# Optimization experiments

Measured on AMD Instinct MI355X. Metric: run time of the kernel, lower is better.

## Reference

```python
import jax, jax.numpy as jnp
import numpy as np

H = 64  # hidden size

def _lstm_last_h(x, W_ih, W_hh, b_ih, b_hh):
    # x: [B, T]; PyTorch LSTM gate order: i, f, g, o (each H wide in 4H axis)
    B, T = x.shape
    # input_size == 1, so x @ W_ih.T == x[..., None] * W_ih[:, 0]
    xproj = x[:, :, None] * W_ih[:, 0][None, None, :] + (b_ih + b_hh)  # [B, T, 4H]
    xproj_t = jnp.swapaxes(xproj, 0, 1)  # [T, B, 4H] for scan over time

    def step(carry, xp_t):
        h, c = carry
        gates = xp_t + h @ W_hh.T  # [B, 4H]
        i = jax.nn.sigmoid(gates[:, 0 * H:1 * H])
        f = jax.nn.sigmoid(gates[:, 1 * H:2 * H])
        g = jnp.tanh(gates[:, 2 * H:3 * H])
        o = jax.nn.sigmoid(gates[:, 3 * H:4 * H])
        c = f * c + i * g
        h = o * jnp.tanh(c)
        return (h, c), None

    h0 = jnp.zeros((B, H), x.dtype)
    c0 = jnp.zeros((B, H), x.dtype)
    (h_last, _), _ = jax.lax.scan(step, (h0, c0), xproj_t)
    return h_last  # [B, H] == lstm_out[:, -1, :]


def setup_inputs() -> dict:
    key = jax.random.key(0)
    ks = jax.random.split(key, 7)
    B, T = 2048, 512
    s_ih = 1.0 / np.sqrt(H)
    return {
        "x": jax.random.normal(ks[0], (B, T), jnp.float32),
        "W_ih": jax.random.uniform(ks[1], (4 * H, 1), jnp.float32, -s_ih, s_ih),
        "W_hh": jax.random.uniform(ks[2], (4 * H, H), jnp.float32, -s_ih, s_ih),
        "b_ih": jax.random.uniform(ks[3], (4 * H,), jnp.float32, -s_ih, s_ih),
        "b_hh": jax.random.uniform(ks[4], (4 * H,), jnp.float32, -s_ih, s_ih),
        "W_d": jax.random.uniform(ks[5], (1, H), jnp.float32, -s_ih, s_ih),
        "b_d": jax.random.uniform(ks[6], (1,), jnp.float32, -s_ih, s_ih),
    }


def reference(x, W_ih, W_hh, b_ih, b_hh, W_d, b_d):
    h_last = _lstm_last_h(x, W_ih, W_hh, b_ih, b_hh)  # [B, H]
    out = h_last @ W_d.T + b_d  # [B, 1]
    return out[:, 0]  # squeeze(1) -> [B]
```

## Files before the change

kernel.cpp:

```cpp
#include <hip/hip_runtime.h>

#define TLEN 512
#define HID  64

typedef _Float16 half8 __attribute__((ext_vector_type(8)));
typedef float    f32x4 __attribute__((ext_vector_type(4)));

__device__ __forceinline__ float rcp_fast(float x) { return __builtin_amdgcn_rcpf(x); }
__device__ __forceinline__ float sigmoid_fast(float x) { return rcp_fast(1.0f + __expf(-x)); }
__device__ __forceinline__ float tanh_fast(float x) { return 1.0f - 2.0f * rcp_fast(__expf(2.0f * x) + 1.0f); }

__global__ __launch_bounds__(512)
void lstm_mfma3(const float* __restrict__ x,
                const float* __restrict__ W_ih,
                const float* __restrict__ W_hh,
                const float* __restrict__ b_ih,
                const float* __restrict__ b_hh,
                const float* __restrict__ W_d,
                const float* __restrict__ b_d,
                float* __restrict__ out) {
    __shared__ __align__(16) float    xs[8][516];
    __shared__ __align__(16) _Float16 hbuf[2][16][72];

    const int tid = threadIdx.x;
    const int L   = tid & 63;
    const int w   = tid >> 6;
    const int r0  = blockIdx.x * 8;

    for (int i = tid; i < 8 * 128; i += 512) {
        const int r = i >> 7, t4 = (i & 127) * 4;
        *(float4*)&xs[r][t4] = *(const float4*)&x[(size_t)(r0 + r) * TLEN + t4];
    }
    for (int i = tid; i < 2 * 16 * 72; i += 512)
        ((_Float16*)hbuf)[i] = (_Float16)0.0f;

    half8 af[2][2];
    {
        const int m = L & 15;
        const int g = m & 3;
        const int kb = (L >> 4) * 8;
#pragma unroll
        for (int tt = 0; tt < 2; ++tt) {
            const int uu = 8 * w + 4 * tt + (m >> 2);
            const float* row = &W_hh[(size_t)(g * HID + uu) * HID];
#pragma unroll
            for (int q = 0; q < 2; ++q) {
                const float* p = row + 32 * q + kb;
                half8 hf;
#pragma unroll
                for (int i = 0; i < 8; ++i) hf[i] = (_Float16)p[i];
                af[tt][q] = hf;
            }
        }
    }

    const int c   = L & 15;
    const int b   = L & 7;
    const int sel = (L >> 3) & 1;
    const int u   = 8 * w + (L >> 4) + 4 * sel;

    float wih[4], bias[4];
#pragma unroll
    for (int g = 0; g < 4; ++g) {
        wih[g]  = W_ih[g * HID + u];
        bias[g] = b_ih[g * HID + u] + b_hh[g * HID + u];
    }

    const float* xrow = &xs[b][0];
    _Float16* hw0 = &hbuf[1][b][u];
    const f32x4 zero = {0.0f, 0.0f, 0.0f, 0.0f};
    float cst = 0.0f;
    int p = 0;

    __syncthreads();

    for (int t = 0; t < TLEN; ++t) {
        const _Float16* hb = &hbuf[p][c][(L >> 4) * 8];
        const float xt = xrow[t];
        half8 b0 = *(const half8*)hb;
        half8 b1 = *(const half8*)(hb + 32);

        f32x4 d0 = __builtin_amdgcn_mfma_f32_16x16x32_f16(af[0][0], b0, zero, 0, 0, 0);
        f32x4 d1 = __builtin_amdgcn_mfma_f32_16x16x32_f16(af[1][0], b0, zero, 0, 0, 0);
        d0 = __builtin_amdgcn_mfma_f32_16x16x32_f16(af[0][1], b1, d0, 0, 0, 0);
        d1 = __builtin_amdgcn_mfma_f32_16x16x32_f16(af[1][1], b1, d1, 0, 0, 0);

        const f32x4 d = sel ? d1 : d0;

        const float ai = d[0] + fmaf(xt, wih[0], bias[0]);
        const float af_ = d[1] + fmaf(xt, wih[1], bias[1]);
        const float ag = d[2] + fmaf(xt, wih[2], bias[2]);
        const float ao = d[3] + fmaf(xt, wih[3], bias[3]);
        const float gi = sigmoid_fast(ai);
        const float gf = sigmoid_fast(af_);
        const float gg = tanh_fast(ag);
        const float go = sigmoid_fast(ao);
        cst = fmaf(gf, cst, gi * gg);
        const float hv = go * tanh_fast(cst);

        const _Float16 hh = (_Float16)hv;
        _Float16* hwp = hw0 + (p ^ 1) * 0 ;
        hbuf[p ^ 1][b][u]     = hh;
        hbuf[p ^ 1][b + 8][u] = hh;
        __syncthreads();
        p ^= 1;
    }

    float pv = (float)hbuf[p][w][L] * W_d[L];
#pragma unroll
    for (int off = 32; off > 0; off >>= 1)
        pv += __shfl_xor(pv, off, 64);
    if (L == 0)
        out[r0 + w] = pv + b_d[0];
}

extern "C" void kernel_launch(void* const* d_in, const int* in_sizes, int n_in,
                              void* d_out, int out_size, void* d_ws, size_t ws_size,
                              hipStream_t stream) {
    const float* x    = (const float*)d_in[0];
    const float* W_ih = (const float*)d_in[1];
    const float* W_hh = (const float*)d_in[2];
    const float* b_ih = (const float*)d_in[3];
    const float* b_hh = (const float*)d_in[4];
    const float* W_d  = (const float*)d_in[5];
    const float* b_d  = (const float*)d_in[6];
    float* out = (float*)d_out;

    dim3 grid(256);
    dim3 block(512);
    lstm_mfma3<<<grid, block, 0, stream>>>(x, W_ih, W_hh, b_ih, b_hh, W_d, b_d, out);
}
```

Measured before the change: 234.2 us.

## Split LSTM batch into 4-row blocks of 4 waves with 16 units each

Each block now handles 4 batch rows with 256 threads (4 waves), and each wave owns 16 hidden units using four MFMA tiles per step instead of two. The grid doubles to 512 blocks, so each __syncthreads in the serial time loop covers fewer waves, and the MFMA B tiles are no longer padded with duplicated rows. The time loop is unrolled by two with fixed ping-pong buffer pointers, which removes the buffer-index arithmetic. The cost is more MFMA work per wave and more register pressure, and a waves-per-eu hint is added to bound occupancy.

```diff
diff --git a/kernel.cpp b/kernel.cpp
--- a/kernel.cpp
+++ b/kernel.cpp
@@ -10,8 +10,8 @@
 __device__ __forceinline__ float sigmoid_fast(float x) { return rcp_fast(1.0f + __expf(-x)); }
 __device__ __forceinline__ float tanh_fast(float x) { return 1.0f - 2.0f * rcp_fast(__expf(2.0f * x) + 1.0f); }
 
-__global__ __launch_bounds__(512)
-void lstm_mfma3(const float* __restrict__ x,
+__global__ __launch_bounds__(256) __attribute__((amdgpu_waves_per_eu(2, 2)))
+void lstm_mfma4(const float* __restrict__ x,
                 const float* __restrict__ W_ih,
                 const float* __restrict__ W_hh,
                 const float* __restrict__ b_ih,
@@ -19,29 +19,29 @@
                 const float* __restrict__ W_d,
                 const float* __restrict__ b_d,
                 float* __restrict__ out) {
-    __shared__ __align__(16) float    xs[8][516];
-    __shared__ __align__(16) _Float16 hbuf[2][16][72];
+    __shared__ __align__(16) float    xs[4][516];
+    __shared__ __align__(16) _Float16 hbuf[2][4][72];
 
     const int tid = threadIdx.x;
     const int L   = tid & 63;
     const int w   = tid >> 6;
-    const int r0  = blockIdx.x * 8;
+    const int r0  = blockIdx.x * 4;
 
-    for (int i = tid; i < 8 * 128; i += 512) {
+    for (int i = tid; i < 4 * 128; i += 256) {
         const int r = i >> 7, t4 = (i & 127) * 4;
         *(float4*)&xs[r][t4] = *(const float4*)&x[(size_t)(r0 + r) * TLEN + t4];
     }
-    for (int i = tid; i < 2 * 16 * 72; i += 512)
+    for (int i = tid; i < 2 * 4 * 72; i += 256)
         ((_Float16*)hbuf)[i] = (_Float16)0.0f;
 
-    half8 af[2][2];
+    half8 af[4][2];
     {
         const int m = L & 15;
         const int g = m & 3;
         const int kb = (L >> 4) * 8;
 #pragma unroll
-        for (int tt = 0; tt < 2; ++tt) {
-            const int uu = 8 * w + 4 * tt + (m >> 2);
+        for (int tt = 0; tt < 4; ++tt) {
+            const int uu = 16 * w + 4 * tt + (m >> 2);
             const float* row = &W_hh[(size_t)(g * HID + uu) * HID];
 #pragma unroll
             for (int q = 0; q < 2; ++q) {
@@ -54,10 +54,9 @@
         }
     }
 
-    const int c   = L & 15;
-    const int b   = L & 7;
-    const int sel = (L >> 3) & 1;
-    const int u   = 8 * w + (L >> 4) + 4 * sel;
+    const int b   = L & 3;
+    const int sel = (L >> 2) & 3;
+    const int u   = 16 * w + 4 * sel + (L >> 4);
 
     float wih[4], bias[4];
 #pragma unroll
@@ -67,46 +66,52 @@
     }
 
     const float* xrow = &xs[b][0];
-    _Float16* hw0 = &hbuf[1][b][u];
+    const int koff = (L >> 4) * 8;
+    const _Float16* h0r = &hbuf[0][b][0];
+    _Float16*       h0w = &hbuf[0][b][0];
+    const _Float16* h1r = &hbuf[1][b][0];
+    _Float16*       h1w = &hbuf[1][b][0];
     const f32x4 zero = {0.0f, 0.0f, 0.0f, 0.0f};
     float cst = 0.0f;
-    int p = 0;
 
     __syncthreads();
 
-    for (int t = 0; t < TLEN; ++t) {
-        const _Float16* hb = &hbuf[p][c][(L >> 4) * 8];
-        const float xt = xrow[t];
-        half8 b0 = *(const half8*)hb;
-        half8 b1 = *(const half8*)(hb + 32);
+    auto step = [&](const _Float16* hin, _Float16* hout, float xt) {
+        half8 b0 = *(const half8*)(hin + koff);
+        half8 b1 = *(const half8*)(hin + koff + 32);
 
         f32x4 d0 = __builtin_amdgcn_mfma_f32_16x16x32_f16(af[0][0], b0, zero, 0, 0, 0);
         f32x4 d1 = __builtin_amdgcn_mfma_f32_16x16x32_f16(af[1][0], b0, zero, 0, 0, 0);
+        f32x4 d2 = __builtin_amdgcn_mfma_f32_16x16x32_f16(af[2][0], b0, zero, 0, 0, 0);
+        f32x4 d3 = __builtin_amdgcn_mfma_f32_16x16x32_f16(af[3][0], b0, zero, 0, 0, 0);
         d0 = __builtin_amdgcn_mfma_f32_16x16x32_f16(af[0][1], b1, d0, 0, 0, 0);
         d1 = __builtin_amdgcn_mfma_f32_16x16x32_f16(af[1][1], b1, d1, 0, 0, 0);
+        d2 = __builtin_amdgcn_mfma_f32_16x16x32_f16(af[2][1], b1, d2, 0, 0, 0);
+        d3 = __builtin_amdgcn_mfma_f32_16x16x32_f16(af[3][1], b1, d3, 0, 0, 0);
 
-        const f32x4 d = sel ? d1 : d0;
+        const f32x4 d = sel == 0 ? d0 : (sel == 1 ? d1 : (sel == 2 ? d2 : d3));
 
-        const float ai = d[0] + fmaf(xt, wih[0], bias[0]);
-        const float af_ = d[1] + fmaf(xt, wih[1], bias[1]);
-        const float ag = d[2] + fmaf(xt, wih[2], bias[2]);
-        const float ao = d[3] + fmaf(xt, wih[3], bias[3]);
+        const float ai  = d[0] + fmaf(xt, wih[0], bias[0]);
+        const float afv = d[1] + fmaf(xt, wih[1], bias[1]);
+        const float ag  = d[2] + fmaf(xt, wih[2], bias[2]);
+        const float ao  = d[3] + fmaf(xt, wih[3], bias[3]);
         const float gi = sigmoid_fast(ai);
-        const float gf = sigmoid_fast(af_);
+        const float gf = sigmoid_fast(afv);
         const float gg = tanh_fast(ag);
         const float go = sigmoid_fast(ao);
         cst = fmaf(gf, cst, gi * gg);
         const float hv = go * tanh_fast(cst);
+        hout[u] = (_Float16)hv;
+    };
 
-        const _Float16 hh = (_Float16)hv;
-        _Float16* hwp = hw0 + (p ^ 1) * 0 ;
-        hbuf[p ^ 1][b][u]     = hh;
-        hbuf[p ^ 1][b + 8][u] = hh;
+    for (int t = 0; t < TLEN; t += 2) {
+        step(h0r, h1w, xrow[t]);
         __syncthreads();
-        p ^= 1;
+        step(h1r, h0w, xrow[t + 1]);
+        __syncthreads();
     }
 
-    float pv = (float)hbuf[p][w][L] * W_d[L];
+    float pv = (float)hbuf[0][w][L] * W_d[L];
 #pragma unroll
     for (int off = 32; off > 0; off >>= 1)
         pv += __shfl_xor(pv, off, 64);
@@ -126,7 +131,7 @@
     const float* b_d  = (const float*)d_in[6];
     float* out = (float*)d_out;
 
-    dim3 grid(256);
-    dim3 block(512);
-    lstm_mfma3<<<grid, block, 0, stream>>>(x, W_ih, W_hh, b_ih, b_hh, W_d, b_d, out);
+    dim3 grid(512);
+    dim3 block(256);
+    lstm_mfma4<<<grid, block, 0, stream>>>(x, W_ih, W_hh, b_ih, b_hh, W_d, b_d, out);
 }
```

New measurement: 235.3 us. About the same (+0.5%).
